# Optimization experiments

Measured on AMD Instinct MI355X. Metric: run time of the kernel, lower is better.

## Reference

```python
import jax, jax.numpy as jnp
import numpy as np

NUM_USER = 100000
NUM_ITEM = 50000
DIM_E = 128
DIM_FEAT = 256
BATCH = 1024
NUM_NEG = 127
TEMP = 2.0
LR_LAMBDA = 0.5
NUM_SAMPLE = 0.5


def _l2norm(x, eps=1e-12):
    n = jnp.linalg.norm(x, axis=1, keepdims=True)
    return x / jnp.maximum(n, eps)


def setup_inputs() -> dict:
    key = jax.random.key(0)
    ks = jax.random.split(key, 9)
    flat = BATCH * (1 + NUM_NEG)
    user_tensor = jax.random.randint(ks[0], (BATCH, 1 + NUM_NEG), 0, NUM_USER, dtype=jnp.int64 if jax.config.jax_enable_x64 else jnp.int32)
    item_tensor = jax.random.randint(ks[1], (BATCH, 1 + NUM_NEG), NUM_USER, NUM_USER + NUM_ITEM, dtype=user_tensor.dtype)
    rand_index = jax.random.randint(ks[2], (int(flat * NUM_SAMPLE),), 0, flat, dtype=user_tensor.dtype)
    id_embedding = jax.random.normal(ks[3], (NUM_USER + NUM_ITEM, DIM_E), jnp.float32) * 0.02
    v_feat = jax.random.normal(ks[4], (NUM_ITEM, DIM_FEAT), jnp.float32)
    W1 = jax.random.normal(ks[5], (DIM_FEAT, 256), jnp.float32) * (1.0 / np.sqrt(DIM_FEAT))
    b1 = jax.random.normal(ks[6], (256,), jnp.float32) * 0.01
    W2 = jax.random.normal(ks[7], (256, DIM_E), jnp.float32) * (1.0 / 16.0)
    b2 = jax.random.normal(ks[8], (DIM_E,), jnp.float32) * 0.01
    return {"user_tensor": user_tensor, "item_tensor": item_tensor, "rand_index": rand_index,
            "id_embedding": id_embedding, "v_feat": v_feat, "W1": W1, "b1": b1, "W2": W2, "b2": b2}


def _contrastive(anchor, all_t):
    # exp(<a,b>/T) grouped into [B, 1+num_neg]; pos is column 0
    score = jnp.exp(jnp.sum(anchor * all_t, axis=1) / TEMP).reshape(-1, 1 + NUM_NEG)
    pos = score[:, 0]
    tot = jnp.sum(score, axis=1)
    return jnp.mean(-jnp.log(pos / tot))


def reference(user_tensor, item_tensor, rand_index, id_embedding, v_feat, W1, b1, W2, b2):
    # encoder: normalize content feats, 2-layer MLP
    feature = _l2norm(v_feat)
    feature = jax.nn.leaky_relu(feature @ W1 + b1)  # slope 0.01, matches torch default
    feature = feature @ W2 + b2                      # [num_item, dim_E]

    pos_flat = jnp.repeat(item_tensor[:, 0:1], 1 + NUM_NEG, axis=1).reshape(-1)
    u_flat = user_tensor.reshape(-1)
    i_flat = item_tensor.reshape(-1)

    all_item_feat = feature[i_flat - NUM_USER]          # [flat, dim_E]
    user_emb = id_embedding[u_flat]
    pos_emb = id_embedding[pos_flat]
    all_item_emb = id_embedding[i_flat]

    head_feat = _l2norm(all_item_feat)
    head_embed = _l2norm(pos_emb)

    # replace a random half of the item embeddings with content features
    all_item_input = all_item_emb.at[rand_index].set(all_item_feat[rand_index])

    c1 = _contrastive(head_embed, head_feat)
    c2 = _contrastive(user_emb, all_item_input)

    reg_loss = (jnp.mean(jnp.sqrt(jnp.sum(user_emb ** 2, axis=1))) +
                jnp.mean(jnp.sqrt(jnp.sum(all_item_emb ** 2, axis=1)))) / 2

    # graph_generator is None -> graph contrastive loss is 0
    total = c1 * LR_LAMBDA + c2 * (1.0 - LR_LAMBDA)
    return total, reg_loss
```

## Files before the change

### kernel.cpp

```cpp
#include <hip/hip_runtime.h>
#include <math.h>

#define NUSER 100000
#define NITEM 50000
#define NID   (NUSER + NITEM)
#define DIM_E 128
#define DIM_F 256
#define BATCH 1024
#define NCOL 128
#define FLAT (BATCH * NCOL)

typedef __attribute__((ext_vector_type(8))) short bf16x8;
typedef __attribute__((ext_vector_type(4))) short bf16x4;
typedef __attribute__((ext_vector_type(4))) float f32x4;

__device__ __forceinline__ float dot4(float4 a, float4 b) {
    return a.x * b.x + a.y * b.y + a.z * b.z + a.w * b.w;
}

__device__ __forceinline__ short f2bf(float x) {
    unsigned u = __float_as_uint(x);
    unsigned r = (u + 0x7FFFu + ((u >> 16) & 1u)) >> 16;
    return (short)r;
}

__device__ __forceinline__ float bf2f(short s) {
    return __uint_as_float(((unsigned)(unsigned short)s) << 16);
}

__global__ __launch_bounds__(256) void prep0_kernel(const float* __restrict__ W1,
                                                    const float* __restrict__ W2,
                                                    short* __restrict__ w1t,
                                                    short* __restrict__ w2t,
                                                    int* __restrict__ flags) {
    int i = blockIdx.x * 256 + threadIdx.x;
    if (i < FLAT) flags[i] = 0;
    if (i < 256 * 256) {
        int n = i >> 8, k = i & 255;
        w1t[i] = f2bf(W1[(size_t)k * 256 + n]);
    } else if (i < 256 * 256 + 128 * 256) {
        int j = i - 256 * 256;
        int n = j >> 8, k = j & 255;
        w2t[j] = f2bf(W2[(size_t)k * 128 + n]);
    }
}

__device__ __forceinline__ void stage_rows(const float4 va[4], int srow, int q,
                                           short* __restrict__ As) {
    float s = 0.f;
#pragma unroll
    for (int c = 0; c < 4; ++c) s += dot4(va[c], va[c]);
#pragma unroll
    for (int off = 8; off >= 1; off >>= 1) s += __shfl_xor(s, off);
    float inv = 1.f / fmaxf(sqrtf(s), 1e-12f);
    bf16x8 p0, p1;
    p0[0] = f2bf(va[0].x * inv); p0[1] = f2bf(va[0].y * inv);
    p0[2] = f2bf(va[0].z * inv); p0[3] = f2bf(va[0].w * inv);
    p0[4] = f2bf(va[1].x * inv); p0[5] = f2bf(va[1].y * inv);
    p0[6] = f2bf(va[1].z * inv); p0[7] = f2bf(va[1].w * inv);
    p1[0] = f2bf(va[2].x * inv); p1[1] = f2bf(va[2].y * inv);
    p1[2] = f2bf(va[2].z * inv); p1[3] = f2bf(va[2].w * inv);
    p1[4] = f2bf(va[3].x * inv); p1[5] = f2bf(va[3].y * inv);
    p1[6] = f2bf(va[3].z * inv); p1[7] = f2bf(va[3].w * inv);
    const int sw = (srow & 7) << 3;
    *(bf16x8*)(&As[srow * 256 + ((q * 16) ^ sw)]) = p0;
    *(bf16x8*)(&As[srow * 256 + ((q * 16 + 8) ^ sw)]) = p1;
}

__global__ __launch_bounds__(512, 2) void fused_prep_kernel(const float* __restrict__ vfeat,
                                                            const short* __restrict__ w1t,
                                                            const float* __restrict__ b1,
                                                            const short* __restrict__ w2t,
                                                            const float* __restrict__ b2,
                                                            short* __restrict__ featout,
                                                            const float* __restrict__ idemb,
                                                            short* __restrict__ idemb_bf,
                                                            float* __restrict__ norms,
                                                            const int* __restrict__ ridx,
                                                            int nridx,
                                                            int* __restrict__ flags) {
    __shared__ __align__(16) short As[32 * 256];
    __shared__ __align__(16) short Hs[32 * 256];
    const int t = threadIdx.x;

    if (blockIdx.x >= 256) {
        const int blk = blockIdx.x - 256;
        if (blk < 128) {
            for (int i = blk * 512 + t; i < nridx; i += 128 * 512) flags[ridx[i]] = 1;
        }
        const int sub = t & 31;
        int row = blk * 16 + (t >> 5);
        for (; row < NID; row += 768 * 16) {
            float4 v = *(const float4*)(idemb + (size_t)row * DIM_E + sub * 4);
            float s = dot4(v, v);
#pragma unroll
            for (int off = 16; off >= 1; off >>= 1) s += __shfl_xor(s, off);
            bf16x4 p;
            p[0] = f2bf(v.x); p[1] = f2bf(v.y); p[2] = f2bf(v.z); p[3] = f2bf(v.w);
            *(bf16x4*)(idemb_bf + (size_t)row * DIM_E + sub * 4) = p;
            if (sub == 0) norms[row] = sqrtf(s);
        }
        return;
    }

    const int w = t >> 6;
    const int l = t & 63;
    const int fr = l & 15;
    const int kg = l >> 4;
    const int srow = t >> 4;
    const int q = t & 15;
    const int NT = (NITEM + 31) / 32;

    bf16x8 B1f[8][2];
    bf16x8 B2f[8];
#pragma unroll
    for (int kc = 0; kc < 8; ++kc) {
#pragma unroll
        for (int ct = 0; ct < 2; ++ct)
            B1f[kc][ct] = *(const bf16x8*)(w1t + (size_t)(w * 32 + ct * 16 + fr) * 256 + kc * 32 + kg * 8);
        B2f[kc] = *(const bf16x8*)(w2t + (size_t)(w * 16 + fr) * 256 + kc * 32 + kg * 8);
    }
    float b1v[2];
    b1v[0] = b1[w * 32 + fr];
    b1v[1] = b1[w * 32 + 16 + fr];
    const float b2v = b2[w * 16 + fr];

    int tile = blockIdx.x;
    {
        float4 va[4];
        int gr = tile * 32 + srow;
        const float* src = vfeat + (size_t)gr * DIM_F + q * 16;
#pragma unroll
        for (int c = 0; c < 4; ++c)
            va[c] = (gr < NITEM) ? *(const float4*)(src + c * 4) : make_float4(0.f, 0.f, 0.f, 0.f);
        stage_rows(va, srow, q, As);
    }
    __syncthreads();

    while (tile < NT) {
        const int tnext = tile + 256;
        float4 vb[4];
        if (tnext < NT) {
            int gr = tnext * 32 + srow;
            const float* src = vfeat + (size_t)gr * DIM_F + q * 16;
#pragma unroll
            for (int c = 0; c < 4; ++c)
                vb[c] = (gr < NITEM) ? *(const float4*)(src + c * 4) : make_float4(0.f, 0.f, 0.f, 0.f);
        }

        {
            f32x4 acc1[2][2];
#pragma unroll
            for (int rt = 0; rt < 2; ++rt)
#pragma unroll
                for (int ct = 0; ct < 2; ++ct) acc1[rt][ct] = (f32x4){0.f, 0.f, 0.f, 0.f};
#pragma unroll
            for (int kc = 0; kc < 8; ++kc) {
                const int kb = kc * 32 + kg * 8;
                bf16x8 af[2];
#pragma unroll
                for (int rt = 0; rt < 2; ++rt) {
                    int row = rt * 16 + fr;
                    af[rt] = *(const bf16x8*)(&As[row * 256 + (kb ^ ((row & 7) << 3))]);
                }
#pragma unroll
                for (int ct = 0; ct < 2; ++ct)
#pragma unroll
                    for (int rt = 0; rt < 2; ++rt)
                        acc1[rt][ct] = __builtin_amdgcn_mfma_f32_16x16x32_bf16(af[rt], B1f[kc][ct], acc1[rt][ct], 0, 0, 0);
            }
#pragma unroll
            for (int rt = 0; rt < 2; ++rt)
#pragma unroll
                for (int ct = 0; ct < 2; ++ct) {
                    int colH = w * 32 + ct * 16 + fr;
#pragma unroll
                    for (int r = 0; r < 4; ++r) {
                        float h = acc1[rt][ct][r] + b1v[ct];
                        h = h > 0.f ? h : 0.01f * h;
                        int row = rt * 16 + kg * 4 + r;
                        Hs[row * 256 + (colH ^ ((row & 7) << 3))] = f2bf(h);
                    }
                }
        }
        __syncthreads();

        {
            f32x4 acc2[2];
            acc2[0] = (f32x4){0.f, 0.f, 0.f, 0.f};
            acc2[1] = (f32x4){0.f, 0.f, 0.f, 0.f};
#pragma unroll
            for (int kc = 0; kc < 8; ++kc) {
                const int kb = kc * 32 + kg * 8;
#pragma unroll
                for (int rt = 0; rt < 2; ++rt) {
                    int row = rt * 16 + fr;
                    bf16x8 hf = *(const bf16x8*)(&Hs[row * 256 + (kb ^ ((row & 7) << 3))]);
                    acc2[rt] = __builtin_amdgcn_mfma_f32_16x16x32_bf16(hf, B2f[kc], acc2[rt], 0, 0, 0);
                }
            }
            const int col = w * 16 + fr;
#pragma unroll
            for (int rt = 0; rt < 2; ++rt)
#pragma unroll
                for (int r = 0; r < 4; ++r) {
                    int row = tile * 32 + rt * 16 + kg * 4 + r;
                    if (row < NITEM) featout[(size_t)row * DIM_E + col] = f2bf(acc2[rt][r] + b2v);
                }
        }

        if (tnext < NT) stage_rows(vb, srow, q, As);
        __syncthreads();
        tile = tnext;
    }
}

__global__ __launch_bounds__(128) void contrast_kernel(const int* __restrict__ user,
                                                       const int* __restrict__ item,
                                                       const int* __restrict__ flags,
                                                       const short* __restrict__ idemb_bf,
                                                       const float* __restrict__ norms,
                                                       const short* __restrict__ feat,
                                                       float* __restrict__ rowpart) {
    __shared__ float pe[128];
    __shared__ float s1s[64], s2s[64], rs[64];
    __shared__ float dpos[2];
    const int row = blockIdx.x >> 1;
    const int part = blockIdx.x & 1;
    const int t = threadIdx.x;

    if (t < 32) {
        int p = item[(size_t)row * NCOL];
        float inv = 1.f / fmaxf(norms[p], 1e-12f);
        bf16x4 v = *(const bf16x4*)(idemb_bf + (size_t)p * DIM_E + t * 4);
        pe[t * 4 + 0] = bf2f(v[0]) * inv;
        pe[t * 4 + 1] = bf2f(v[1]) * inv;
        pe[t * 4 + 2] = bf2f(v[2]) * inv;
        pe[t * 4 + 3] = bf2f(v[3]) * inv;
    }
    __syncthreads();

    const int el = t >> 1;
    const int e = part * 64 + el;
    const int h = t & 1;
    const size_t j = (size_t)row * NCOL + e;
    const int u = user[j];
    const int it = item[j];
    const int fl = flags[j];
    const short* up = idemb_bf + (size_t)u * DIM_E + h * 64;
    const short* ip = idemb_bf + (size_t)it * DIM_E + h * 64;
    const short* fp = feat + (size_t)(it - NUSER) * DIM_E + h * 64;

    bf16x8 ub[8], fb[8], xb[8];
#pragma unroll
    for (int i = 0; i < 8; ++i) { ub[i] = ((const bf16x8*)up)[i]; fb[i] = ((const bf16x8*)fp)[i]; }
    if (fl) {
#pragma unroll
        for (int i = 0; i < 8; ++i) xb[i] = fb[i];
    } else {
#pragma unroll
        for (int i = 0; i < 8; ++i) xb[i] = ((const bf16x8*)ip)[i];
    }
    float nu = norms[u];
    float ni = norms[it];

    float sf = 0.f, dpf = 0.f, dux = 0.f;
#pragma unroll
    for (int i = 0; i < 8; ++i) {
        float4 p0 = *(const float4*)(&pe[h * 64 + i * 8]);
        float4 p1 = *(const float4*)(&pe[h * 64 + i * 8 + 4]);
        float pk[8] = {p0.x, p0.y, p0.z, p0.w, p1.x, p1.y, p1.z, p1.w};
#pragma unroll
        for (int k = 0; k < 8; ++k) {
            float fv = bf2f(fb[i][k]);
            float uv = bf2f(ub[i][k]);
            float xv = bf2f(xb[i][k]);
            sf += fv * fv;
            dpf += pk[k] * fv;
            dux += uv * xv;
        }
    }
    sf += __shfl_xor(sf, 1);
    dpf += __shfl_xor(dpf, 1);
    dux += __shfl_xor(dux, 1);

    if (h == 0) {
        float fnorm = fmaxf(sqrtf(sf), 1e-12f);
        float d1 = dpf / fnorm * 0.5f;
        float d2 = dux * 0.5f;
        s1s[el] = expf(d1);
        s2s[el] = expf(d2);
        rs[el] = nu + ni;
        if (e == 0) { dpos[0] = d1; dpos[1] = d2; }
    }
    __syncthreads();

    if (t < 32) {
        float a1 = s1s[t] + s1s[t + 32];
        float a2 = s2s[t] + s2s[t + 32];
        float a3 = rs[t] + rs[t + 32];
#pragma unroll
        for (int off = 16; off >= 1; off >>= 1) {
            a1 += __shfl_xor(a1, off);
            a2 += __shfl_xor(a2, off);
            a3 += __shfl_xor(a3, off);
        }
        if (t == 0) {
            float* dst = rowpart + (size_t)blockIdx.x * 6;
            dst[0] = a1;
            dst[1] = a2;
            dst[2] = a3;
            if (part == 0) { dst[3] = dpos[0]; dst[4] = dpos[1]; }
        }
    }
}

__global__ __launch_bounds__(256) void finalize_kernel(const float* __restrict__ rowpart,
                                                       float* __restrict__ out) {
    float c1 = 0.f, c2 = 0.f, rg = 0.f;
    for (int r = threadIdx.x; r < BATCH; r += 256) {
        const float* p0 = rowpart + (size_t)(r * 2) * 6;
        const float* p1 = rowpart + (size_t)(r * 2 + 1) * 6;
        float A1 = p0[0] + p1[0];
        float A2 = p0[1] + p1[1];
        c1 += logf(A1) - p0[3];
        c2 += logf(A2) - p0[4];
        rg += p0[2] + p1[2];
    }
#pragma unroll
    for (int off = 32; off >= 1; off >>= 1) {
        c1 += __shfl_xor(c1, off);
        c2 += __shfl_xor(c2, off);
        rg += __shfl_xor(rg, off);
    }
    __shared__ float buf[4][3];
    int wid = threadIdx.x >> 6, lane = threadIdx.x & 63;
    if (lane == 0) { buf[wid][0] = c1; buf[wid][1] = c2; buf[wid][2] = rg; }
    __syncthreads();
    if (threadIdx.x == 0) {
        float C1 = buf[0][0] + buf[1][0] + buf[2][0] + buf[3][0];
        float C2 = buf[0][1] + buf[1][1] + buf[2][1] + buf[3][1];
        float R  = buf[0][2] + buf[1][2] + buf[2][2] + buf[3][2];
        out[0] = 0.5f * (C1 / (float)BATCH) + 0.5f * (C2 / (float)BATCH);
        out[1] = 0.5f * (R / (float)FLAT);
    }
}

extern "C" void kernel_launch(void* const* d_in, const int* in_sizes, int n_in,
                              void* d_out, int out_size, void* d_ws, size_t ws_size,
                              hipStream_t stream) {
    const int* user = (const int*)d_in[0];
    const int* item = (const int*)d_in[1];
    const int* ridx = (const int*)d_in[2];
    const float* idemb = (const float*)d_in[3];
    const float* vfeat = (const float*)d_in[4];
    const float* W1 = (const float*)d_in[5];
    const float* b1 = (const float*)d_in[6];
    const float* W2 = (const float*)d_in[7];
    const float* b2 = (const float*)d_in[8];
    float* out = (float*)d_out;

    char* ws = (char*)d_ws;
    short* feat_bf  = (short*)(ws);
    short* idemb_bf = (short*)(ws + 12800000);
    float* norms    = (float*)(ws + 51200000);
    int*   flags    = (int*)  (ws + 51800000);
    float* rowpart  = (float*)(ws + 52324288);
    short* w1t      = (short*)(ws + 52373440);
    short* w2t      = (short*)(ws + 52504512);

    const int nridx = in_sizes[2];

    prep0_kernel<<<dim3(512), dim3(256), 0, stream>>>(W1, W2, w1t, w2t, flags);
    fused_prep_kernel<<<dim3(1024), dim3(512), 0, stream>>>(vfeat, w1t, b1, w2t, b2, feat_bf,
                                                            idemb, idemb_bf, norms,
                                                            ridx, nridx, flags);
    contrast_kernel<<<dim3(2 * BATCH), dim3(128), 0, stream>>>(user, item, flags,
                                                               idemb_bf, norms, feat_bf, rowpart);
    finalize_kernel<<<dim3(1), dim3(256), 0, stream>>>(rowpart, out);
}
```

Before: 78.19 us.

## Split feature normalization into streaming kernel and run MLP on pre-normalized bf16 input

The fused kernel that both L2-normalized v_feat rows and ran the MFMA MLP is split in two. A streaming kernel now normalizes v_feat into a bf16 workspace buffer alongside the id-embedding conversion and flag setting. A separate MLP kernel then loads the pre-normalized bf16 rows directly into shared memory. This removes the per-tile normalization and fp32 loads from the MFMA loop and spreads the streaming work across more blocks. The cost is an extra kernel launch and an extra write and read of a 25.6 MB intermediate buffer, and the MLP no longer overlaps with the id-embedding streaming.

```diff
diff --git a/kernel.cpp b/kernel.cpp
--- a/kernel.cpp
+++ b/kernel.cpp
@@ -9,6 +9,7 @@
 #define BATCH 1024
 #define NCOL 128
 #define FLAT (BATCH * NCOL)
+#define NT   ((NITEM + 31) / 32)
 
 typedef __attribute__((ext_vector_type(8))) short bf16x8;
 typedef __attribute__((ext_vector_type(4))) short bf16x4;
@@ -45,52 +46,37 @@
     }
 }
 
-__device__ __forceinline__ void stage_rows(const float4 va[4], int srow, int q,
-                                           short* __restrict__ As) {
-    float s = 0.f;
-#pragma unroll
-    for (int c = 0; c < 4; ++c) s += dot4(va[c], va[c]);
-#pragma unroll
-    for (int off = 8; off >= 1; off >>= 1) s += __shfl_xor(s, off);
-    float inv = 1.f / fmaxf(sqrtf(s), 1e-12f);
-    bf16x8 p0, p1;
-    p0[0] = f2bf(va[0].x * inv); p0[1] = f2bf(va[0].y * inv);
-    p0[2] = f2bf(va[0].z * inv); p0[3] = f2bf(va[0].w * inv);
-    p0[4] = f2bf(va[1].x * inv); p0[5] = f2bf(va[1].y * inv);
-    p0[6] = f2bf(va[1].z * inv); p0[7] = f2bf(va[1].w * inv);
-    p1[0] = f2bf(va[2].x * inv); p1[1] = f2bf(va[2].y * inv);
-    p1[2] = f2bf(va[2].z * inv); p1[3] = f2bf(va[2].w * inv);
-    p1[4] = f2bf(va[3].x * inv); p1[5] = f2bf(va[3].y * inv);
-    p1[6] = f2bf(va[3].z * inv); p1[7] = f2bf(va[3].w * inv);
-    const int sw = (srow & 7) << 3;
-    *(bf16x8*)(&As[srow * 256 + ((q * 16) ^ sw)]) = p0;
-    *(bf16x8*)(&As[srow * 256 + ((q * 16 + 8) ^ sw)]) = p1;
-}
-
-__global__ __launch_bounds__(512, 2) void fused_prep_kernel(const float* __restrict__ vfeat,
-                                                            const short* __restrict__ w1t,
-                                                            const float* __restrict__ b1,
-                                                            const short* __restrict__ w2t,
-                                                            const float* __restrict__ b2,
-                                                            short* __restrict__ featout,
-                                                            const float* __restrict__ idemb,
-                                                            short* __restrict__ idemb_bf,
-                                                            float* __restrict__ norms,
-                                                            const int* __restrict__ ridx,
-                                                            int nridx,
-                                                            int* __restrict__ flags) {
-    __shared__ __align__(16) short As[32 * 256];
-    __shared__ __align__(16) short Hs[32 * 256];
+__global__ __launch_bounds__(256) void stream_kernel(const float* __restrict__ vfeat,
+                                                     short* __restrict__ vfeatn,
+                                                     const float* __restrict__ idemb,
+                                                     short* __restrict__ idemb_bf,
+                                                     float* __restrict__ norms,
+                                                     const int* __restrict__ ridx,
+                                                     int nridx,
+                                                     int* __restrict__ flags) {
     const int t = threadIdx.x;
-
-    if (blockIdx.x >= 256) {
-        const int blk = blockIdx.x - 256;
+    if (blockIdx.x < 768) {
+        const int wv = blockIdx.x * 4 + (t >> 6);
+        const int l = t & 63;
+        for (int row = wv; row < NITEM; row += 3072) {
+            float4 v = *(const float4*)(vfeat + (size_t)row * DIM_F + l * 4);
+            float s = dot4(v, v);
+#pragma unroll
+            for (int off = 32; off >= 1; off >>= 1) s += __shfl_xor(s, off);
+            float inv = 1.f / fmaxf(sqrtf(s), 1e-12f);
+            bf16x4 p;
+            p[0] = f2bf(v.x * inv); p[1] = f2bf(v.y * inv);
+            p[2] = f2bf(v.z * inv); p[3] = f2bf(v.w * inv);
+            *(bf16x4*)(vfeatn + (size_t)row * DIM_F + l * 4) = p;
+        }
+    } else {
+        const int blk = blockIdx.x - 768;
         if (blk < 128) {
-            for (int i = blk * 512 + t; i < nridx; i += 128 * 512) flags[ridx[i]] = 1;
+            for (int i = blk * 256 + t; i < nridx; i += 128 * 256) flags[ridx[i]] = 1;
         }
         const int sub = t & 31;
-        int row = blk * 16 + (t >> 5);
-        for (; row < NID; row += 768 * 16) {
+        int row = blk * 8 + (t >> 5);
+        for (; row < NID; row += 1280 * 8) {
             float4 v = *(const float4*)(idemb + (size_t)row * DIM_E + sub * 4);
             float s = dot4(v, v);
 #pragma unroll
@@ -100,16 +86,25 @@
             *(bf16x4*)(idemb_bf + (size_t)row * DIM_E + sub * 4) = p;
             if (sub == 0) norms[row] = sqrtf(s);
         }
-        return;
-    }
-
+    }
+}
+
+__global__ __launch_bounds__(512, 2) void mlp_mfma_kernel(const short* __restrict__ vfeatn,
+                                                          const short* __restrict__ w1t,
+                                                          const float* __restrict__ b1,
+                                                          const short* __restrict__ w2t,
+                                                          const float* __restrict__ b2,
+                                                          short* __restrict__ featout) {
+    __shared__ __align__(16) short As[32 * 256];
+    __shared__ __align__(16) short Hs[32 * 256];
+    const int t = threadIdx.x;
     const int w = t >> 6;
     const int l = t & 63;
     const int fr = l & 15;
     const int kg = l >> 4;
     const int srow = t >> 4;
     const int q = t & 15;
-    const int NT = (NITEM + 31) / 32;
+    const int sw = (srow & 7) << 3;
 
     bf16x8 B1f[8][2];
     bf16x8 B2f[8];
@@ -127,25 +122,26 @@
 
     int tile = blockIdx.x;
     {
-        float4 va[4];
+        bf16x8 r0 = {0,0,0,0,0,0,0,0}, r1 = {0,0,0,0,0,0,0,0};
         int gr = tile * 32 + srow;
-        const float* src = vfeat + (size_t)gr * DIM_F + q * 16;
-#pragma unroll
-        for (int c = 0; c < 4; ++c)
-            va[c] = (gr < NITEM) ? *(const float4*)(src + c * 4) : make_float4(0.f, 0.f, 0.f, 0.f);
-        stage_rows(va, srow, q, As);
+        if (gr < NITEM) {
+            const bf16x8* s = (const bf16x8*)(vfeatn + (size_t)gr * DIM_F + q * 16);
+            r0 = s[0]; r1 = s[1];
+        }
+        *(bf16x8*)(&As[srow * 256 + ((q * 16) ^ sw)]) = r0;
+        *(bf16x8*)(&As[srow * 256 + ((q * 16 + 8) ^ sw)]) = r1;
     }
     __syncthreads();
 
     while (tile < NT) {
         const int tnext = tile + 256;
-        float4 vb[4];
+        bf16x8 n0 = {0,0,0,0,0,0,0,0}, n1 = {0,0,0,0,0,0,0,0};
         if (tnext < NT) {
             int gr = tnext * 32 + srow;
-            const float* src = vfeat + (size_t)gr * DIM_F + q * 16;
-#pragma unroll
-            for (int c = 0; c < 4; ++c)
-                vb[c] = (gr < NITEM) ? *(const float4*)(src + c * 4) : make_float4(0.f, 0.f, 0.f, 0.f);
+            if (gr < NITEM) {
+                const bf16x8* s = (const bf16x8*)(vfeatn + (size_t)gr * DIM_F + q * 16);
+                n0 = s[0]; n1 = s[1];
+            }
         }
 
         {
@@ -209,7 +205,10 @@
                 }
         }
 
-        if (tnext < NT) stage_rows(vb, srow, q, As);
+        if (tnext < NT) {
+            *(bf16x8*)(&As[srow * 256 + ((q * 16) ^ sw)]) = n0;
+            *(bf16x8*)(&As[srow * 256 + ((q * 16 + 8) ^ sw)]) = n1;
+        }
         __syncthreads();
         tile = tnext;
     }
@@ -363,18 +362,19 @@
     char* ws = (char*)d_ws;
     short* feat_bf  = (short*)(ws);
     short* idemb_bf = (short*)(ws + 12800000);
-    float* norms    = (float*)(ws + 51200000);
-    int*   flags    = (int*)  (ws + 51800000);
-    float* rowpart  = (float*)(ws + 52324288);
-    short* w1t      = (short*)(ws + 52373440);
-    short* w2t      = (short*)(ws + 52504512);
+    short* vfeatn   = (short*)(ws + 51200000);
+    float* norms    = (float*)(ws + 76800000);
+    int*   flags    = (int*)  (ws + 77400000);
+    float* rowpart  = (float*)(ws + 77924288);
+    short* w1t      = (short*)(ws + 77973440);
+    short* w2t      = (short*)(ws + 78104512);
 
     const int nridx = in_sizes[2];
 
     prep0_kernel<<<dim3(512), dim3(256), 0, stream>>>(W1, W2, w1t, w2t, flags);
-    fused_prep_kernel<<<dim3(1024), dim3(512), 0, stream>>>(vfeat, w1t, b1, w2t, b2, feat_bf,
-                                                            idemb, idemb_bf, norms,
-                                                            ridx, nridx, flags);
+    stream_kernel<<<dim3(2048), dim3(256), 0, stream>>>(vfeat, vfeatn, idemb, idemb_bf,
+                                                        norms, ridx, nridx, flags);
+    mlp_mfma_kernel<<<dim3(256), dim3(512), 0, stream>>>(vfeatn, w1t, b1, w2t, b2, feat_bf);
     contrast_kernel<<<dim3(2 * BATCH), dim3(128), 0, stream>>>(user, item, flags,
                                                                idemb_bf, norms, feat_bf, rowpart);
     finalize_kernel<<<dim3(1), dim3(256), 0, stream>>>(rowpart, out);
```

After: 83.55 us. +6.9%, slower.
